# Performance work log

Hardware: AMD Instinct MI355X
Metric: run time of the kernel (lower is better)

## Reference

```python
import jax, jax.numpy as jnp
import numpy as np

H = 128          # hidden_dim
L = 3            # n_layers
G = 128          # num graphs in batch
BN_EPS = 1e-5


def setup_inputs() -> dict:
    key = jax.random.key(0)
    ks = jax.random.split(key, 16)
    N, E, ND, ED = 2048, 8192, 32, 16
    s = lambda k, shape, fan: jax.random.normal(k, shape, dtype=jnp.float32) / np.sqrt(fan)
    return {
        "x": jax.random.normal(ks[0], (N, ND), dtype=jnp.float32),
        "edge_index": jax.random.randint(ks[1], (2, E), 0, N),
        "edge_attr": jax.random.normal(ks[2], (E, ED), dtype=jnp.float32),
        "batch": jnp.sort(jax.random.randint(ks[3], (N,), 0, G)),
        "node_W": s(ks[4], (ND, H), ND),
        "node_b": jnp.zeros((H,), jnp.float32),
        "edge_W": s(ks[5], (L, ED, H * H), ED),
        "edge_b": jnp.zeros((L, H * H), jnp.float32),
        "root_W": s(ks[6], (L, H, H), H),
        "conv_bias": jnp.zeros((L, H), jnp.float32),
        "bn_gamma": jnp.ones((L, H), jnp.float32),
        "bn_beta": jnp.zeros((L, H), jnp.float32),
        "cls_W1": s(ks[7], (H, 64), H),
        "cls_b1": jnp.zeros((64,), jnp.float32),
        "cls_W2": s(ks[8], (64, 1), 64),
        "cls_b2": jnp.zeros((1,), jnp.float32),
    }


def _segment_mean(vals, ids, num_segments):
    ssum = jax.ops.segment_sum(vals, ids, num_segments=num_segments)
    cnt = jax.ops.segment_sum(jnp.ones((vals.shape[0],), vals.dtype), ids,
                              num_segments=num_segments)
    return ssum / jnp.maximum(cnt, 1.0)[:, None]


def reference(x, edge_index, edge_attr, batch, node_W, node_b, edge_W, edge_b,
              root_W, conv_bias, bn_gamma, bn_beta, cls_W1, cls_b1, cls_W2, cls_b2):
    N = x.shape[0]
    src, dst = edge_index[0], edge_index[1]
    h = x @ node_W + node_b                                   # [N, H]
    for l in range(L):
        # edge-conditioned weights: [E, H, H]
        W = (edge_attr @ edge_W[l] + edge_b[l]).reshape(-1, H, H)
        msg = jnp.einsum('ei,eio->eo', h[src], W)             # gather + per-edge matmul
        agg = _segment_mean(msg, dst, N)                      # scatter-mean
        x_new = h @ root_W[l] + agg + conv_bias[l]
        # BatchNorm (batch statistics, training-mode math)
        mu = jnp.mean(x_new, axis=0)
        var = jnp.var(x_new, axis=0)
        x_new = (x_new - mu) * jax.lax.rsqrt(var + BN_EPS) * bn_gamma[l] + bn_beta[l]
        x_new = jax.nn.relu(x_new)                            # dropout omitted (eval)
        h = h + x_new                                         # residual
    g = _segment_mean(h, batch, G)                            # global mean pool [G, H]
    out = jax.nn.relu(g @ cls_W1 + cls_b1) @ cls_W2 + cls_b2  # classifier
    return out.squeeze(-1)                                    # [G]
```

## Files before the change

kernel.cpp:

```cpp
#include <hip/hip_runtime.h>
#include <cstddef>
#include <cstdint>

#define H 128
#define EDIM 16
#define NLAYER 3
#define NSLICE 18
#define WCOLS (NSLICE * H)
#define PCOLS (EDIM * H)
#define TM 64
#define TN 64
#define TK 16

typedef unsigned short ushort_t;
typedef unsigned int uint_t;
typedef __attribute__((ext_vector_type(8))) short bf16x8;
typedef __attribute__((ext_vector_type(4))) float f32x4;

__device__ __forceinline__ ushort_t f2bf(float f) {
    uint_t u = __builtin_bit_cast(uint_t, f);
    u += 0x7fffu + ((u >> 16) & 1u);
    return (ushort_t)(u >> 16);
}
__device__ __forceinline__ float bf_lo(uint_t u) {
    return __builtin_bit_cast(float, u << 16);
}
__device__ __forceinline__ float bf_hi(uint_t u) {
    return __builtin_bit_cast(float, u & 0xffff0000u);
}

__global__ __launch_bounds__(256) void setup_kernel(
    const int* __restrict__ dst, const int* __restrict__ batch,
    int* __restrict__ hist, float* __restrict__ cntG, int E, int N,
    const float* __restrict__ eW, const float* __restrict__ eb,
    const float* __restrict__ rW, ushort_t* __restrict__ Wt)
{
    if (blockIdx.x < 32) {
        int t = blockIdx.x * 256 + threadIdx.x;
        if (t < E) atomicAdd(&hist[dst[t]], 1);
        if (t < N) atomicAdd(&cntG[batch[t]], 1.f);
        return;
    }
    __shared__ ushort_t tile[128][136];
    const int b = blockIdx.x - 32;
    const int l = b / NSLICE, s = b % NSLICE;
    const float* S = (s < 16) ? (eW + ((size_t)l * 16 + s) * (H * H))
                   : (s == 16 ? (eb + (size_t)l * H * H)
                              : (rW + (size_t)l * H * H));
    const int t = threadIdx.x;
    const int k = t >> 1, o0 = (t & 1) * 64;
#pragma unroll
    for (int j = 0; j < 64; j += 4) {
        float4 v = *(const float4*)&S[(size_t)k * H + o0 + j];
        tile[k][o0 + j + 0] = f2bf(v.x);
        tile[k][o0 + j + 1] = f2bf(v.y);
        tile[k][o0 + j + 2] = f2bf(v.z);
        tile[k][o0 + j + 3] = f2bf(v.w);
    }
    __syncthreads();
    const int n = t >> 1, k0 = (t & 1) * 64;
    ushort_t* outp = Wt + ((size_t)l * WCOLS + s * H + n) * H + k0;
#pragma unroll 8
    for (int j = 0; j < 64; ++j) outp[j] = tile[k0 + j][n];
}

__global__ __launch_bounds__(256) void scan_kernel(
    const int* __restrict__ hist, int* __restrict__ offs, int N)
{
    __shared__ int part[256];
    const int t = threadIdx.x;
    const int base = t * 8;
    int v[8], loc[8], s = 0;
#pragma unroll
    for (int j = 0; j < 8; ++j) v[j] = hist[base + j];
#pragma unroll
    for (int j = 0; j < 8; ++j) { loc[j] = s; s += v[j]; }
    part[t] = s;
    __syncthreads();
    for (int off = 1; off < 256; off <<= 1) {
        int x = (t >= off) ? part[t - off] : 0;
        __syncthreads();
        part[t] += x;
        __syncthreads();
    }
    const int boff = (t == 0) ? 0 : part[t - 1];
#pragma unroll
    for (int j = 0; j < 8; ++j) offs[base + j] = boff + loc[j];
    if (t == 255) offs[N] = boff + s;
}

__global__ void scatter_kernel(const int* __restrict__ dst,
                               const int* __restrict__ offs,
                               int* __restrict__ fill, int* __restrict__ eord, int E)
{
    const int e = blockIdx.x * 256 + threadIdx.x;
    if (e >= E) return;
    const int d = dst[e];
    const int pos = offs[d] + atomicAdd(&fill[d], 1);
    eord[pos] = e;
}

__global__ __launch_bounds__(256) void gemm_embed(
    const float* __restrict__ A, const float* __restrict__ B,
    const float* __restrict__ bias, float* __restrict__ C,
    ushort_t* __restrict__ Cbf, int M, int K, int N)
{
    __shared__ float As[TK][TM + 4];
    __shared__ float Bs[TK][TN + 4];
    const int bm = blockIdx.y * TM;
    const int bn = blockIdx.x * TN;
    const int tid = threadIdx.x;
    const int tx = tid & 15;
    const int ty = tid >> 4;

    float acc[4][4];
#pragma unroll
    for (int i = 0; i < 4; ++i)
#pragma unroll
        for (int j = 0; j < 4; ++j) acc[i][j] = 0.f;

    const int ka = tid & 15, ma = tid >> 4;
    const int nb = tid & 63, kb = tid >> 6;

    for (int k0 = 0; k0 < K; k0 += TK) {
#pragma unroll
        for (int r = 0; r < 4; ++r)
            As[ka][ma + 16 * r] = A[(size_t)(bm + ma + 16 * r) * K + (k0 + ka)];
#pragma unroll
        for (int r = 0; r < 4; ++r)
            Bs[kb + 4 * r][nb] = B[(size_t)(k0 + kb + 4 * r) * N + bn + nb];
        __syncthreads();
#pragma unroll
        for (int kk = 0; kk < TK; ++kk) {
            const float4 a4 = *(const float4*)&As[kk][ty * 4];
            const float4 b4 = *(const float4*)&Bs[kk][tx * 4];
            const float a[4] = {a4.x, a4.y, a4.z, a4.w};
            const float b[4] = {b4.x, b4.y, b4.z, b4.w};
#pragma unroll
            for (int i = 0; i < 4; ++i)
#pragma unroll
                for (int j = 0; j < 4; ++j)
                    acc[i][j] = fmaf(a[i], b[j], acc[i][j]);
        }
        __syncthreads();
    }

#pragma unroll
    for (int i = 0; i < 4; ++i) {
        const int row = bm + ty * 4 + i;
        float4 v;
        v.x = acc[i][0] + bias[(bn + tx * 4 + 0) & 127];
        v.y = acc[i][1] + bias[(bn + tx * 4 + 1) & 127];
        v.z = acc[i][2] + bias[(bn + tx * 4 + 2) & 127];
        v.w = acc[i][3] + bias[(bn + tx * 4 + 3) & 127];
        *(float4*)&C[(size_t)row * N + bn + tx * 4] = v;
        ushort_t* o = &Cbf[(size_t)row * N + bn + tx * 4];
        o[0] = f2bf(v.x); o[1] = f2bf(v.y); o[2] = f2bf(v.z); o[3] = f2bf(v.w);
    }
}

__global__ __launch_bounds__(256) void mfma_gemm(
    const ushort_t* __restrict__ hbf, const ushort_t* __restrict__ Wt,
    ushort_t* __restrict__ Pb, float* __restrict__ QR)
{
    __shared__ ushort_t As[64][136];
    __shared__ ushort_t Bs[64][136];
    const int tid = threadIdx.x;
    const int v0 = blockIdx.y * 64;
    const int n0 = blockIdx.x * 64;

    {
        const int row = tid >> 2, col0 = (tid & 3) * 32;
        const ushort_t* ga = hbf + (size_t)(v0 + row) * H + col0;
        const ushort_t* gb = Wt + (size_t)(n0 + row) * H + col0;
#pragma unroll
        for (int j = 0; j < 32; j += 8) {
            *(uint4*)&As[row][col0 + j] = *(const uint4*)(ga + j);
            *(uint4*)&Bs[row][col0 + j] = *(const uint4*)(gb + j);
        }
    }
    __syncthreads();

    const int wave = tid >> 6, lane = tid & 63;
    const int l15 = lane & 15, kg = lane >> 4;
    const int mrow = wave * 16 + l15;

    f32x4 acc0 = {0.f, 0.f, 0.f, 0.f};
    f32x4 acc1 = {0.f, 0.f, 0.f, 0.f};
    f32x4 acc2 = {0.f, 0.f, 0.f, 0.f};
    f32x4 acc3 = {0.f, 0.f, 0.f, 0.f};

#pragma unroll
    for (int s = 0; s < 4; ++s) {
        const int k = s * 32 + kg * 8;
        bf16x8 a = *(const bf16x8*)&As[mrow][k];
        bf16x8 b0 = *(const bf16x8*)&Bs[0 * 16 + l15][k];
        bf16x8 b1 = *(const bf16x8*)&Bs[1 * 16 + l15][k];
        bf16x8 b2 = *(const bf16x8*)&Bs[2 * 16 + l15][k];
        bf16x8 b3 = *(const bf16x8*)&Bs[3 * 16 + l15][k];
        acc0 = __builtin_amdgcn_mfma_f32_16x16x32_bf16(a, b0, acc0, 0, 0, 0);
        acc1 = __builtin_amdgcn_mfma_f32_16x16x32_bf16(a, b1, acc1, 0, 0, 0);
        acc2 = __builtin_amdgcn_mfma_f32_16x16x32_bf16(a, b2, acc2, 0, 0, 0);
        acc3 = __builtin_amdgcn_mfma_f32_16x16x32_bf16(a, b3, acc3, 0, 0, 0);
    }

    const int slice = n0 >> 7;
    const int lo = n0 & 127;
    const int row0 = v0 + wave * 16 + kg * 4;
    if (slice < 16) {
        ushort_t* op = Pb + (size_t)row0 * PCOLS + slice * H + lo + l15;
#pragma unroll
        for (int r = 0; r < 4; ++r) {
            op[(size_t)r * PCOLS + 0]  = f2bf(acc0[r]);
            op[(size_t)r * PCOLS + 16] = f2bf(acc1[r]);
            op[(size_t)r * PCOLS + 32] = f2bf(acc2[r]);
            op[(size_t)r * PCOLS + 48] = f2bf(acc3[r]);
        }
    } else {
        float* op = QR + (size_t)row0 * 256 + (slice - 16) * H + lo + l15;
#pragma unroll
        for (int r = 0; r < 4; ++r) {
            op[(size_t)r * 256 + 0]  = acc0[r];
            op[(size_t)r * 256 + 16] = acc1[r];
            op[(size_t)r * 256 + 32] = acc2[r];
            op[(size_t)r * 256 + 48] = acc3[r];
        }
    }
}

__global__ __launch_bounds__(256) void edge_stats(
    const ushort_t* __restrict__ Pb, const float* __restrict__ QR,
    const float* __restrict__ ea, const int* __restrict__ srcArr,
    const int* __restrict__ offs, const int* __restrict__ hist,
    const int* __restrict__ eord, const float* __restrict__ conv_b,
    float* __restrict__ xnew, float* __restrict__ bnS, float* __restrict__ bnQ)
{
    __shared__ float sS[4][H];
    __shared__ float sQ[4][H];
    const int tid = threadIdx.x;
    const int sb = tid >> 6;
    const int o2 = tid & 63;
    const int v = blockIdx.x * 4 + sb;

    const int st = offs[v];
    const int deg = hist[v];
    float m0 = 0.f, m1 = 0.f;
    for (int k = 0; k < deg; ++k) {
        const int e = eord[st + k];
        const int s = srcArr[e];
        const float* eap = ea + (size_t)e * EDIM;
        const float4 w0 = *(const float4*)(eap + 0);
        const float4 w1 = *(const float4*)(eap + 4);
        const float4 w2 = *(const float4*)(eap + 8);
        const float4 w3 = *(const float4*)(eap + 12);
        const float w[16] = {w0.x, w0.y, w0.z, w0.w, w1.x, w1.y, w1.z, w1.w,
                             w2.x, w2.y, w2.z, w2.w, w3.x, w3.y, w3.z, w3.w};
        const uint_t* prow = (const uint_t*)(Pb + (size_t)s * PCOLS) + o2;
        const float2 q2 = *(const float2*)(QR + (size_t)s * 256 + 2 * o2);
        m0 += q2.x;
        m1 += q2.y;
#pragma unroll
        for (int d = 0; d < EDIM; ++d) {
            const uint_t u = prow[(size_t)d * 64];
            m0 = fmaf(w[d], bf_lo(u), m0);
            m1 = fmaf(w[d], bf_hi(u), m1);
        }
    }
    const float rc = 1.0f / (float)(deg > 0 ? deg : 1);
    const float2 rt = *(const float2*)(QR + (size_t)v * 256 + H + 2 * o2);
    const float2 cb = *(const float2*)(conv_b + 2 * o2);
    const float val0 = m0 * rc + rt.x + cb.x;
    const float val1 = m1 * rc + rt.y + cb.y;
    *(float2*)(xnew + (size_t)v * H + 2 * o2) = make_float2(val0, val1);
    sS[sb][2 * o2] = val0; sS[sb][2 * o2 + 1] = val1;
    sQ[sb][2 * o2] = val0 * val0; sQ[sb][2 * o2 + 1] = val1 * val1;
    __syncthreads();
    if (tid < H) {
        const float s4 = sS[0][tid] + sS[1][tid] + sS[2][tid] + sS[3][tid];
        const float q4 = sQ[0][tid] + sQ[1][tid] + sQ[2][tid] + sQ[3][tid];
        atomicAdd(&bnS[tid], s4);
        atomicAdd(&bnQ[tid], q4);
    }
}

__global__ __launch_bounds__(256) void bn_apply(
    float* __restrict__ h, ushort_t* __restrict__ hbf,
    const float* __restrict__ xnew,
    const float* __restrict__ bnS, const float* __restrict__ bnQ,
    const float* __restrict__ gamma, const float* __restrict__ beta,
    const int* __restrict__ batch, float* __restrict__ gsum, int N, int last)
{
    const int idx = blockIdx.x * 256 + threadIdx.x;
    const int c = idx & 127;
    const int v = idx >> 7;
    const float invN = 1.0f / (float)N;
    const float mu = bnS[c] * invN;
    const float var = bnQ[c] * invN - mu * mu;
    const float val = (xnew[idx] - mu) * rsqrtf(var + 1e-5f) * gamma[c] + beta[c];
    const float hn = h[idx] + fmaxf(val, 0.f);
    h[idx] = hn;
    hbf[idx] = f2bf(hn);
    if (last) atomicAdd(&gsum[batch[v] * H + c], hn);
}

__global__ void classifier_kernel(
    const float* __restrict__ gsum, const float* __restrict__ cntG,
    const float* __restrict__ W1, const float* __restrict__ b1,
    const float* __restrict__ W2, const float* __restrict__ b2,
    float* __restrict__ out)
{
    const int g = blockIdx.x;
    const int j = threadIdx.x;
    const float rc = 1.0f / fmaxf(cntG[g], 1.0f);
    float acc = b1[j];
#pragma unroll 8
    for (int i = 0; i < H; ++i)
        acc = fmaf(gsum[g * H + i] * rc, W1[i * 64 + j], acc);
    float pv = fmaxf(acc, 0.f) * W2[j];
#pragma unroll
    for (int off = 32; off > 0; off >>= 1)
        pv += __shfl_down(pv, off);
    if (j == 0) out[g] = pv + b2[0];
}

extern "C" void kernel_launch(void* const* d_in, const int* in_sizes, int n_in,
                              void* d_out, int out_size, void* d_ws, size_t ws_size,
                              hipStream_t stream)
{
    const float* x      = (const float*)d_in[0];
    const int*   eidx   = (const int*)  d_in[1];
    const float* eattr  = (const float*)d_in[2];
    const int*   batch  = (const int*)  d_in[3];
    const float* node_W = (const float*)d_in[4];
    const float* node_b = (const float*)d_in[5];
    const float* edge_W = (const float*)d_in[6];
    const float* edge_b = (const float*)d_in[7];
    const float* root_W = (const float*)d_in[8];
    const float* conv_b = (const float*)d_in[9];
    const float* gamma  = (const float*)d_in[10];
    const float* beta   = (const float*)d_in[11];
    const float* W1     = (const float*)d_in[12];
    const float* b1     = (const float*)d_in[13];
    const float* W2     = (const float*)d_in[14];
    const float* b2     = (const float*)d_in[15];
    float* out = (float*)d_out;

    const int N = in_sizes[0] / 32;
    const int E = in_sizes[1] / 2;
    const int G = out_size;

    int* hist   = (int*)d_ws;
    int* fill   = hist + N;
    float* cntG = (float*)(fill + N);
    float* bnS  = cntG + G;
    float* bnQ  = bnS + NLAYER * H;
    float* gsum = bnQ + NLAYER * H;
    int* offs   = (int*)(gsum + (size_t)G * H);
    int* eord   = offs + (N + 16);
    float* h    = (float*)(eord + E);
    float* xnew = h + (size_t)N * H;
    ushort_t* hbf = (ushort_t*)(xnew + (size_t)N * H);
    ushort_t* Wt  = hbf + (size_t)N * H;
    ushort_t* Pb  = Wt + (size_t)NLAYER * WCOLS * H;
    float* QR   = (float*)(Pb + (size_t)N * PCOLS);

    const size_t zbytes = (size_t)(2 * N) * 4
                        + ((size_t)G + 2 * NLAYER * H + (size_t)G * H) * 4;
    hipMemsetAsync(hist, 0, zbytes, stream);

    const int* src = eidx;
    const int* dst = eidx + E;

    setup_kernel<<<32 + NLAYER * NSLICE, 256, 0, stream>>>(
        dst, batch, hist, cntG, E, N, edge_W, edge_b, root_W, Wt);
    scan_kernel<<<1, 256, 0, stream>>>(hist, offs, N);
    scatter_kernel<<<E / 256, 256, 0, stream>>>(dst, offs, fill, eord, E);

    gemm_embed<<<dim3(H / TN, N / TM), 256, 0, stream>>>(
        x, node_W, node_b, h, hbf, N, 32, H);

    for (int l = 0; l < NLAYER; ++l) {
        mfma_gemm<<<dim3(WCOLS / 64, N / 64), 256, 0, stream>>>(
            hbf, Wt + (size_t)l * WCOLS * H, Pb, QR);
        edge_stats<<<N / 4, 256, 0, stream>>>(
            Pb, QR, eattr, src, offs, hist, eord,
            conv_b + (size_t)l * H, xnew, bnS + l * H, bnQ + l * H);
        bn_apply<<<(N * H) / 256, 256, 0, stream>>>(
            h, hbf, xnew, bnS + l * H, bnQ + l * H,
            gamma + (size_t)l * H, beta + (size_t)l * H,
            batch, gsum, N, l == NLAYER - 1);
    }

    classifier_kernel<<<G, 64, 0, stream>>>(gsum, cntG, W1, b1, W2, b2, out);
}
```

Before: 205.7 us.

## Reassociate edge conv as per-node aggregation then single K=2304 GEMM

The per-layer pipeline changes order. Instead of computing h times every edge-weight slice for all nodes and then gathering those products per edge, each node now builds a vector of edge-attribute-weighted sums of its neighbours' h, plus the plain neighbour sum and its own h, all in bf16. That vector is then multiplied once against the concatenated weights, with K=2304, with the BN statistics reduced in the same kernel. The histogram, scan, scatter, embedding GEMM, weight transpose and zeroing are merged into one setup kernel, which removes the memset and several launches. The conv bias is dropped because batch-norm mean subtraction cancels it. Risks: the new GEMM runs only N/16 blocks, each streaming the full weight matrix through an unpipelined K loop, and U is staged as a large bf16 buffer.

```diff
diff --git a/kernel.cpp b/kernel.cpp
--- a/kernel.cpp
+++ b/kernel.cpp
@@ -5,12 +5,8 @@
 #define H 128
 #define EDIM 16
 #define NLAYER 3
+#define KU 2304
 #define NSLICE 18
-#define WCOLS (NSLICE * H)
-#define PCOLS (EDIM * H)
-#define TM 64
-#define TN 64
-#define TK 16
 
 typedef unsigned short ushort_t;
 typedef unsigned int uint_t;
@@ -22,232 +18,174 @@
     u += 0x7fffu + ((u >> 16) & 1u);
     return (ushort_t)(u >> 16);
 }
-__device__ __forceinline__ float bf_lo(uint_t u) {
-    return __builtin_bit_cast(float, u << 16);
-}
-__device__ __forceinline__ float bf_hi(uint_t u) {
-    return __builtin_bit_cast(float, u & 0xffff0000u);
+__device__ __forceinline__ uint_t pack2(float a, float b) {
+    return (uint_t)f2bf(a) | ((uint_t)f2bf(b) << 16);
 }
 
 __global__ __launch_bounds__(256) void setup_kernel(
     const int* __restrict__ dst, const int* __restrict__ batch,
-    int* __restrict__ hist, float* __restrict__ cntG, int E, int N,
+    const float* __restrict__ x, const float* __restrict__ node_W,
+    const float* __restrict__ node_b,
     const float* __restrict__ eW, const float* __restrict__ eb,
-    const float* __restrict__ rW, ushort_t* __restrict__ Wt)
-{
-    if (blockIdx.x < 32) {
-        int t = blockIdx.x * 256 + threadIdx.x;
-        if (t < E) atomicAdd(&hist[dst[t]], 1);
-        if (t < N) atomicAdd(&cntG[batch[t]], 1.f);
+    const float* __restrict__ rW,
+    int* __restrict__ offs, int* __restrict__ deg, int* __restrict__ eord,
+    float* __restrict__ cntG, float* __restrict__ bnS, float* __restrict__ bnQ,
+    float* __restrict__ gsum, float* __restrict__ h, ushort_t* __restrict__ Wt2,
+    int E, int N, int G)
+{
+    alignas(16) __shared__ unsigned char smem[34816];
+    const int b = blockIdx.x;
+    const int t = threadIdx.x;
+    const int NBe = (N / 64) * 2;
+
+    if (b == 0) {
+        int* sh = (int*)smem;
+        int* part = sh + 2048;
+        for (int i = t; i < N; i += 256) sh[i] = 0;
+        __syncthreads();
+        for (int e = t; e < E; e += 256) atomicAdd(&sh[dst[e]], 1);
+        __syncthreads();
+        const int base = t * 8;
+        int v[8], loc[8], s = 0;
+#pragma unroll
+        for (int j = 0; j < 8; ++j) v[j] = (base + j < N) ? sh[base + j] : 0;
+#pragma unroll
+        for (int j = 0; j < 8; ++j) { loc[j] = s; s += v[j]; }
+        part[t] = s;
+        __syncthreads();
+        for (int off = 1; off < 256; off <<= 1) {
+            int xp = (t >= off) ? part[t - off] : 0;
+            __syncthreads();
+            part[t] += xp;
+            __syncthreads();
+        }
+        const int boff = (t == 0) ? 0 : part[t - 1];
+#pragma unroll
+        for (int j = 0; j < 8; ++j) {
+            if (base + j < N) {
+                deg[base + j] = v[j];
+                offs[base + j] = boff + loc[j];
+            }
+        }
+        if (t == 255) offs[N] = boff + s;
+        __syncthreads();
+        for (int i = t; i < N; i += 256) sh[i] = offs[i];
+        __syncthreads();
+        for (int e = t; e < E; e += 256) {
+            const int d = dst[e];
+            const int pos = atomicAdd(&sh[d], 1);
+            eord[pos] = e;
+        }
         return;
     }
-    __shared__ ushort_t tile[128][136];
-    const int b = blockIdx.x - 32;
-    const int l = b / NSLICE, s = b % NSLICE;
-    const float* S = (s < 16) ? (eW + ((size_t)l * 16 + s) * (H * H))
-                   : (s == 16 ? (eb + (size_t)l * H * H)
-                              : (rW + (size_t)l * H * H));
-    const int t = threadIdx.x;
-    const int k = t >> 1, o0 = (t & 1) * 64;
-#pragma unroll
-    for (int j = 0; j < 64; j += 4) {
-        float4 v = *(const float4*)&S[(size_t)k * H + o0 + j];
-        tile[k][o0 + j + 0] = f2bf(v.x);
-        tile[k][o0 + j + 1] = f2bf(v.y);
-        tile[k][o0 + j + 2] = f2bf(v.z);
-        tile[k][o0 + j + 3] = f2bf(v.w);
-    }
-    __syncthreads();
-    const int n = t >> 1, k0 = (t & 1) * 64;
-    ushort_t* outp = Wt + ((size_t)l * WCOLS + s * H + n) * H + k0;
+
+    if (b <= NLAYER * NSLICE) {
+        ushort_t* tile = (ushort_t*)smem;
+        const int bb = b - 1;
+        const int l = bb / NSLICE, s = bb % NSLICE;
+        const float* S = (s < 16) ? (eW + ((size_t)l * 16 + s) * (H * H))
+                       : (s == 16 ? (eb + (size_t)l * H * H)
+                                  : (rW + (size_t)l * H * H));
+        const int k = t >> 1, o0 = (t & 1) * 64;
+#pragma unroll
+        for (int j = 0; j < 64; j += 4) {
+            float4 v = *(const float4*)&S[(size_t)k * H + o0 + j];
+            tile[k * 136 + o0 + j + 0] = f2bf(v.x);
+            tile[k * 136 + o0 + j + 1] = f2bf(v.y);
+            tile[k * 136 + o0 + j + 2] = f2bf(v.z);
+            tile[k * 136 + o0 + j + 3] = f2bf(v.w);
+        }
+        __syncthreads();
+        const int n = t >> 1, k0 = (t & 1) * 64;
+        ushort_t* outp = Wt2 + ((size_t)(l * H + n)) * KU + s * H + k0;
 #pragma unroll 8
-    for (int j = 0; j < 64; ++j) outp[j] = tile[k0 + j][n];
-}
-
-__global__ __launch_bounds__(256) void scan_kernel(
-    const int* __restrict__ hist, int* __restrict__ offs, int N)
-{
-    __shared__ int part[256];
-    const int t = threadIdx.x;
-    const int base = t * 8;
-    int v[8], loc[8], s = 0;
-#pragma unroll
-    for (int j = 0; j < 8; ++j) v[j] = hist[base + j];
-#pragma unroll
-    for (int j = 0; j < 8; ++j) { loc[j] = s; s += v[j]; }
-    part[t] = s;
-    __syncthreads();
-    for (int off = 1; off < 256; off <<= 1) {
-        int x = (t >= off) ? part[t - off] : 0;
-        __syncthreads();
-        part[t] += x;
-        __syncthreads();
-    }
-    const int boff = (t == 0) ? 0 : part[t - 1];
-#pragma unroll
-    for (int j = 0; j < 8; ++j) offs[base + j] = boff + loc[j];
-    if (t == 255) offs[N] = boff + s;
-}
-
-__global__ void scatter_kernel(const int* __restrict__ dst,
-                               const int* __restrict__ offs,
-                               int* __restrict__ fill, int* __restrict__ eord, int E)
-{
-    const int e = blockIdx.x * 256 + threadIdx.x;
-    if (e >= E) return;
-    const int d = dst[e];
-    const int pos = offs[d] + atomicAdd(&fill[d], 1);
-    eord[pos] = e;
-}
-
-__global__ __launch_bounds__(256) void gemm_embed(
-    const float* __restrict__ A, const float* __restrict__ B,
-    const float* __restrict__ bias, float* __restrict__ C,
-    ushort_t* __restrict__ Cbf, int M, int K, int N)
-{
-    __shared__ float As[TK][TM + 4];
-    __shared__ float Bs[TK][TN + 4];
-    const int bm = blockIdx.y * TM;
-    const int bn = blockIdx.x * TN;
-    const int tid = threadIdx.x;
-    const int tx = tid & 15;
-    const int ty = tid >> 4;
-
-    float acc[4][4];
-#pragma unroll
-    for (int i = 0; i < 4; ++i)
-#pragma unroll
-        for (int j = 0; j < 4; ++j) acc[i][j] = 0.f;
-
-    const int ka = tid & 15, ma = tid >> 4;
-    const int nb = tid & 63, kb = tid >> 6;
-
-    for (int k0 = 0; k0 < K; k0 += TK) {
-#pragma unroll
-        for (int r = 0; r < 4; ++r)
-            As[ka][ma + 16 * r] = A[(size_t)(bm + ma + 16 * r) * K + (k0 + ka)];
-#pragma unroll
-        for (int r = 0; r < 4; ++r)
-            Bs[kb + 4 * r][nb] = B[(size_t)(k0 + kb + 4 * r) * N + bn + nb];
-        __syncthreads();
-#pragma unroll
-        for (int kk = 0; kk < TK; ++kk) {
-            const float4 a4 = *(const float4*)&As[kk][ty * 4];
-            const float4 b4 = *(const float4*)&Bs[kk][tx * 4];
-            const float a[4] = {a4.x, a4.y, a4.z, a4.w};
-            const float b[4] = {b4.x, b4.y, b4.z, b4.w};
-#pragma unroll
-            for (int i = 0; i < 4; ++i)
-#pragma unroll
-                for (int j = 0; j < 4; ++j)
-                    acc[i][j] = fmaf(a[i], b[j], acc[i][j]);
-        }
-        __syncthreads();
-    }
-
-#pragma unroll
-    for (int i = 0; i < 4; ++i) {
-        const int row = bm + ty * 4 + i;
-        float4 v;
-        v.x = acc[i][0] + bias[(bn + tx * 4 + 0) & 127];
-        v.y = acc[i][1] + bias[(bn + tx * 4 + 1) & 127];
-        v.z = acc[i][2] + bias[(bn + tx * 4 + 2) & 127];
-        v.w = acc[i][3] + bias[(bn + tx * 4 + 3) & 127];
-        *(float4*)&C[(size_t)row * N + bn + tx * 4] = v;
-        ushort_t* o = &Cbf[(size_t)row * N + bn + tx * 4];
-        o[0] = f2bf(v.x); o[1] = f2bf(v.y); o[2] = f2bf(v.z); o[3] = f2bf(v.w);
-    }
-}
-
-__global__ __launch_bounds__(256) void mfma_gemm(
-    const ushort_t* __restrict__ hbf, const ushort_t* __restrict__ Wt,
-    ushort_t* __restrict__ Pb, float* __restrict__ QR)
-{
-    __shared__ ushort_t As[64][136];
-    __shared__ ushort_t Bs[64][136];
-    const int tid = threadIdx.x;
-    const int v0 = blockIdx.y * 64;
-    const int n0 = blockIdx.x * 64;
+        for (int j = 0; j < 64; ++j) outp[j] = tile[(k0 + j) * 136 + n];
+        return;
+    }
+
+    if (b <= NLAYER * NSLICE + NBe) {
+        float* As = (float*)smem;
+        float* Bs = As + 16 * 68;
+        const int tt = b - (NLAYER * NSLICE + 1);
+        const int bm = (tt >> 1) * 64;
+        const int bn = (tt & 1) * 64;
+        const int tx = t & 15, ty = t >> 4;
+        float acc[4][4];
+#pragma unroll
+        for (int i = 0; i < 4; ++i)
+#pragma unroll
+            for (int j = 0; j < 4; ++j) acc[i][j] = 0.f;
+        const int ka = t & 15, ma = t >> 4;
+        const int nb = t & 63, kb = t >> 6;
+        for (int k0 = 0; k0 < 32; k0 += 16) {
+#pragma unroll
+            for (int r = 0; r < 4; ++r)
+                As[ka * 68 + ma + 16 * r] = x[(size_t)(bm + ma + 16 * r) * 32 + (k0 + ka)];
+#pragma unroll
+            for (int r = 0; r < 4; ++r)
+                Bs[(kb + 4 * r) * 68 + nb] = node_W[(size_t)(k0 + kb + 4 * r) * H + bn + nb];
+            __syncthreads();
+#pragma unroll
+            for (int kk = 0; kk < 16; ++kk) {
+                const float4 a4 = *(const float4*)&As[kk * 68 + ty * 4];
+                const float4 b4 = *(const float4*)&Bs[kk * 68 + tx * 4];
+                const float a[4] = {a4.x, a4.y, a4.z, a4.w};
+                const float bv[4] = {b4.x, b4.y, b4.z, b4.w};
+#pragma unroll
+                for (int i = 0; i < 4; ++i)
+#pragma unroll
+                    for (int j = 0; j < 4; ++j)
+                        acc[i][j] = fmaf(a[i], bv[j], acc[i][j]);
+            }
+            __syncthreads();
+        }
+#pragma unroll
+        for (int i = 0; i < 4; ++i) {
+            const int row = bm + ty * 4 + i;
+            float4 v;
+            v.x = acc[i][0] + node_b[bn + tx * 4 + 0];
+            v.y = acc[i][1] + node_b[bn + tx * 4 + 1];
+            v.z = acc[i][2] + node_b[bn + tx * 4 + 2];
+            v.w = acc[i][3] + node_b[bn + tx * 4 + 3];
+            *(float4*)&h[(size_t)row * H + bn + tx * 4] = v;
+        }
+        return;
+    }
 
     {
-        const int row = tid >> 2, col0 = (tid & 3) * 32;
-        const ushort_t* ga = hbf + (size_t)(v0 + row) * H + col0;
-        const ushort_t* gb = Wt + (size_t)(n0 + row) * H + col0;
-#pragma unroll
-        for (int j = 0; j < 32; j += 8) {
-            *(uint4*)&As[row][col0 + j] = *(const uint4*)(ga + j);
-            *(uint4*)&Bs[row][col0 + j] = *(const uint4*)(gb + j);
-        }
-    }
-    __syncthreads();
-
-    const int wave = tid >> 6, lane = tid & 63;
-    const int l15 = lane & 15, kg = lane >> 4;
-    const int mrow = wave * 16 + l15;
-
-    f32x4 acc0 = {0.f, 0.f, 0.f, 0.f};
-    f32x4 acc1 = {0.f, 0.f, 0.f, 0.f};
-    f32x4 acc2 = {0.f, 0.f, 0.f, 0.f};
-    f32x4 acc3 = {0.f, 0.f, 0.f, 0.f};
-
-#pragma unroll
-    for (int s = 0; s < 4; ++s) {
-        const int k = s * 32 + kg * 8;
-        bf16x8 a = *(const bf16x8*)&As[mrow][k];
-        bf16x8 b0 = *(const bf16x8*)&Bs[0 * 16 + l15][k];
-        bf16x8 b1 = *(const bf16x8*)&Bs[1 * 16 + l15][k];
-        bf16x8 b2 = *(const bf16x8*)&Bs[2 * 16 + l15][k];
-        bf16x8 b3 = *(const bf16x8*)&Bs[3 * 16 + l15][k];
-        acc0 = __builtin_amdgcn_mfma_f32_16x16x32_bf16(a, b0, acc0, 0, 0, 0);
-        acc1 = __builtin_amdgcn_mfma_f32_16x16x32_bf16(a, b1, acc1, 0, 0, 0);
-        acc2 = __builtin_amdgcn_mfma_f32_16x16x32_bf16(a, b2, acc2, 0, 0, 0);
-        acc3 = __builtin_amdgcn_mfma_f32_16x16x32_bf16(a, b3, acc3, 0, 0, 0);
-    }
-
-    const int slice = n0 >> 7;
-    const int lo = n0 & 127;
-    const int row0 = v0 + wave * 16 + kg * 4;
-    if (slice < 16) {
-        ushort_t* op = Pb + (size_t)row0 * PCOLS + slice * H + lo + l15;
-#pragma unroll
-        for (int r = 0; r < 4; ++r) {
-            op[(size_t)r * PCOLS + 0]  = f2bf(acc0[r]);
-            op[(size_t)r * PCOLS + 16] = f2bf(acc1[r]);
-            op[(size_t)r * PCOLS + 32] = f2bf(acc2[r]);
-            op[(size_t)r * PCOLS + 48] = f2bf(acc3[r]);
-        }
-    } else {
-        float* op = QR + (size_t)row0 * 256 + (slice - 16) * H + lo + l15;
-#pragma unroll
-        for (int r = 0; r < 4; ++r) {
-            op[(size_t)r * 256 + 0]  = acc0[r];
-            op[(size_t)r * 256 + 16] = acc1[r];
-            op[(size_t)r * 256 + 32] = acc2[r];
-            op[(size_t)r * 256 + 48] = acc3[r];
-        }
-    }
-}
-
-__global__ __launch_bounds__(256) void edge_stats(
-    const ushort_t* __restrict__ Pb, const float* __restrict__ QR,
-    const float* __restrict__ ea, const int* __restrict__ srcArr,
-    const int* __restrict__ offs, const int* __restrict__ hist,
-    const int* __restrict__ eord, const float* __restrict__ conv_b,
-    float* __restrict__ xnew, float* __restrict__ bnS, float* __restrict__ bnQ)
-{
-    __shared__ float sS[4][H];
-    __shared__ float sQ[4][H];
+        const int zcount = G * H + 2 * NLAYER * H + G;
+        for (int i = t; i < zcount; i += 256) {
+            if (i < G * H) gsum[i] = 0.f;
+            else if (i < G * H + NLAYER * H) bnS[i - G * H] = 0.f;
+            else if (i < G * H + 2 * NLAYER * H) bnQ[i - G * H - NLAYER * H] = 0.f;
+            else cntG[i - G * H - 2 * NLAYER * H] = 0.f;
+        }
+        __syncthreads();
+        for (int v = t; v < N; v += 256) atomicAdd(&cntG[batch[v]], 1.f);
+    }
+}
+
+__global__ __launch_bounds__(256) void ubuild_kernel(
+    const float* __restrict__ h, const float* __restrict__ ea,
+    const int* __restrict__ src, const int* __restrict__ offs,
+    const int* __restrict__ deg, const int* __restrict__ eord,
+    ushort_t* __restrict__ Ub, int N)
+{
     const int tid = threadIdx.x;
     const int sb = tid >> 6;
-    const int o2 = tid & 63;
+    const int j = tid & 63;
     const int v = blockIdx.x * 4 + sb;
+    if (v >= N) return;
+
+    float u[17][2];
+#pragma unroll
+    for (int d = 0; d < 17; ++d) { u[d][0] = 0.f; u[d][1] = 0.f; }
 
     const int st = offs[v];
-    const int deg = hist[v];
-    float m0 = 0.f, m1 = 0.f;
-    for (int k = 0; k < deg; ++k) {
+    const int dg = deg[v];
+    for (int k = 0; k < dg; ++k) {
         const int e = eord[st + k];
-        const int s = srcArr[e];
+        const int s = src[e];
         const float* eap = ea + (size_t)e * EDIM;
         const float4 w0 = *(const float4*)(eap + 0);
         const float4 w1 = *(const float4*)(eap + 4);
@@ -255,37 +193,89 @@
         const float4 w3 = *(const float4*)(eap + 12);
         const float w[16] = {w0.x, w0.y, w0.z, w0.w, w1.x, w1.y, w1.z, w1.w,
                              w2.x, w2.y, w2.z, w2.w, w3.x, w3.y, w3.z, w3.w};
-        const uint_t* prow = (const uint_t*)(Pb + (size_t)s * PCOLS) + o2;
-        const float2 q2 = *(const float2*)(QR + (size_t)s * 256 + 2 * o2);
-        m0 += q2.x;
-        m1 += q2.y;
-#pragma unroll
-        for (int d = 0; d < EDIM; ++d) {
-            const uint_t u = prow[(size_t)d * 64];
-            m0 = fmaf(w[d], bf_lo(u), m0);
-            m1 = fmaf(w[d], bf_hi(u), m1);
-        }
-    }
-    const float rc = 1.0f / (float)(deg > 0 ? deg : 1);
-    const float2 rt = *(const float2*)(QR + (size_t)v * 256 + H + 2 * o2);
-    const float2 cb = *(const float2*)(conv_b + 2 * o2);
-    const float val0 = m0 * rc + rt.x + cb.x;
-    const float val1 = m1 * rc + rt.y + cb.y;
-    *(float2*)(xnew + (size_t)v * H + 2 * o2) = make_float2(val0, val1);
-    sS[sb][2 * o2] = val0; sS[sb][2 * o2 + 1] = val1;
-    sQ[sb][2 * o2] = val0 * val0; sQ[sb][2 * o2 + 1] = val1 * val1;
-    __syncthreads();
-    if (tid < H) {
-        const float s4 = sS[0][tid] + sS[1][tid] + sS[2][tid] + sS[3][tid];
-        const float q4 = sQ[0][tid] + sQ[1][tid] + sQ[2][tid] + sQ[3][tid];
-        atomicAdd(&bnS[tid], s4);
-        atomicAdd(&bnQ[tid], q4);
+        const float2 h2 = *(const float2*)&h[(size_t)s * H + 2 * j];
+        u[16][0] += h2.x;
+        u[16][1] += h2.y;
+#pragma unroll
+        for (int d = 0; d < 16; ++d) {
+            u[d][0] = fmaf(w[d], h2.x, u[d][0]);
+            u[d][1] = fmaf(w[d], h2.y, u[d][1]);
+        }
+    }
+    const float rc = 1.0f / (float)(dg > 0 ? dg : 1);
+    uint_t* outp = (uint_t*)(Ub + (size_t)v * KU) + j;
+#pragma unroll
+    for (int d = 0; d < 17; ++d)
+        outp[(size_t)d * 64] = pack2(u[d][0] * rc, u[d][1] * rc);
+    const float2 hv = *(const float2*)&h[(size_t)v * H + 2 * j];
+    outp[(size_t)17 * 64] = pack2(hv.x, hv.y);
+}
+
+__global__ __launch_bounds__(256) void gemm_stats(
+    const ushort_t* __restrict__ Ub, const ushort_t* __restrict__ Wt2l,
+    float* __restrict__ xnew, float* __restrict__ bnS, float* __restrict__ bnQ)
+{
+    __shared__ ushort_t As[16][136];
+    __shared__ ushort_t Bs[128][136];
+    const int tid = threadIdx.x;
+    const int m0 = blockIdx.x * 16;
+    const int wave = tid >> 6, lane = tid & 63;
+    const int l15 = lane & 15, quad = lane >> 4;
+
+    f32x4 acc0 = {0.f, 0.f, 0.f, 0.f};
+    f32x4 acc1 = {0.f, 0.f, 0.f, 0.f};
+
+    for (int c = 0; c < KU / 128; ++c) {
+        {
+            const int row = tid >> 4, pos = (tid & 15) * 8;
+            *(uint4*)&As[row][pos] =
+                *(const uint4*)&Ub[(size_t)(m0 + row) * KU + c * 128 + pos];
+        }
+#pragma unroll
+        for (int r = 0; r < 8; ++r) {
+            const int idx = tid + r * 256;
+            const int row = idx >> 4, pos = (idx & 15) * 8;
+            *(uint4*)&Bs[row][pos] =
+                *(const uint4*)&Wt2l[(size_t)row * KU + c * 128 + pos];
+        }
+        __syncthreads();
+#pragma unroll
+        for (int ks = 0; ks < 4; ++ks) {
+            const int k = ks * 32 + quad * 8;
+            bf16x8 a  = *(const bf16x8*)&As[l15][k];
+            bf16x8 b0 = *(const bf16x8*)&Bs[wave * 16 + l15][k];
+            bf16x8 b1 = *(const bf16x8*)&Bs[(wave + 4) * 16 + l15][k];
+            acc0 = __builtin_amdgcn_mfma_f32_16x16x32_bf16(a, b0, acc0, 0, 0, 0);
+            acc1 = __builtin_amdgcn_mfma_f32_16x16x32_bf16(a, b1, acc1, 0, 0, 0);
+        }
+        __syncthreads();
+    }
+
+    float s0 = 0.f, q0 = 0.f, s1 = 0.f, q1 = 0.f;
+#pragma unroll
+    for (int r = 0; r < 4; ++r) {
+        const int row = m0 + quad * 4 + r;
+        const float v0 = acc0[r];
+        const float v1 = acc1[r];
+        xnew[(size_t)row * H + wave * 16 + l15] = v0;
+        xnew[(size_t)row * H + (wave + 4) * 16 + l15] = v1;
+        s0 += v0; q0 += v0 * v0;
+        s1 += v1; q1 += v1 * v1;
+    }
+    s0 += __shfl_down(s0, 32); s0 += __shfl_down(s0, 16);
+    q0 += __shfl_down(q0, 32); q0 += __shfl_down(q0, 16);
+    s1 += __shfl_down(s1, 32); s1 += __shfl_down(s1, 16);
+    q1 += __shfl_down(q1, 32); q1 += __shfl_down(q1, 16);
+    if (quad == 0) {
+        atomicAdd(&bnS[wave * 16 + l15], s0);
+        atomicAdd(&bnQ[wave * 16 + l15], q0);
+        atomicAdd(&bnS[(wave + 4) * 16 + l15], s1);
+        atomicAdd(&bnQ[(wave + 4) * 16 + l15], q1);
     }
 }
 
 __global__ __launch_bounds__(256) void bn_apply(
-    float* __restrict__ h, ushort_t* __restrict__ hbf,
-    const float* __restrict__ xnew,
+    float* __restrict__ h, const float* __restrict__ xnew,
     const float* __restrict__ bnS, const float* __restrict__ bnQ,
     const float* __restrict__ gamma, const float* __restrict__ beta,
     const int* __restrict__ batch, float* __restrict__ gsum, int N, int last)
@@ -299,7 +289,6 @@
     const float val = (xnew[idx] - mu) * rsqrtf(var + 1e-5f) * gamma[c] + beta[c];
     const float hn = h[idx] + fmaxf(val, 0.f);
     h[idx] = hn;
-    hbf[idx] = f2bf(hn);
     if (last) atomicAdd(&gsum[batch[v] * H + c], hn);
 }
 
@@ -336,7 +325,6 @@
     const float* edge_W = (const float*)d_in[6];
     const float* edge_b = (const float*)d_in[7];
     const float* root_W = (const float*)d_in[8];
-    const float* conv_b = (const float*)d_in[9];
     const float* gamma  = (const float*)d_in[10];
     const float* beta   = (const float*)d_in[11];
     const float* W1     = (const float*)d_in[12];
@@ -349,44 +337,35 @@
     const int E = in_sizes[1] / 2;
     const int G = out_size;
 
-    int* hist   = (int*)d_ws;
-    int* fill   = hist + N;
-    float* cntG = (float*)(fill + N);
+    const int* src = eidx;
+    const int* dst = eidx + E;
+
+    int* offs  = (int*)d_ws;
+    int* deg   = offs + (N + 16);
+    int* eord  = deg + N;
+    float* cntG = (float*)(eord + E);
     float* bnS  = cntG + G;
     float* bnQ  = bnS + NLAYER * H;
     float* gsum = bnQ + NLAYER * H;
-    int* offs   = (int*)(gsum + (size_t)G * H);
-    int* eord   = offs + (N + 16);
-    float* h    = (float*)(eord + E);
+    float* h    = gsum + (size_t)G * H;
     float* xnew = h + (size_t)N * H;
-    ushort_t* hbf = (ushort_t*)(xnew + (size_t)N * H);
-    ushort_t* Wt  = hbf + (size_t)N * H;
-    ushort_t* Pb  = Wt + (size_t)NLAYER * WCOLS * H;
-    float* QR   = (float*)(Pb + (size_t)N * PCOLS);
-
-    const size_t zbytes = (size_t)(2 * N) * 4
-                        + ((size_t)G + 2 * NLAYER * H + (size_t)G * H) * 4;
-    hipMemsetAsync(hist, 0, zbytes, stream);
-
-    const int* src = eidx;
-    const int* dst = eidx + E;
-
-    setup_kernel<<<32 + NLAYER * NSLICE, 256, 0, stream>>>(
-        dst, batch, hist, cntG, E, N, edge_W, edge_b, root_W, Wt);
-    scan_kernel<<<1, 256, 0, stream>>>(hist, offs, N);
-    scatter_kernel<<<E / 256, 256, 0, stream>>>(dst, offs, fill, eord, E);
-
-    gemm_embed<<<dim3(H / TN, N / TM), 256, 0, stream>>>(
-        x, node_W, node_b, h, hbf, N, 32, H);
+    ushort_t* Wt2 = (ushort_t*)(xnew + (size_t)N * H);
+    ushort_t* Ub  = Wt2 + (size_t)NLAYER * H * KU;
+
+    const int NBe = (N / 64) * 2;
+    const int nsetup = 1 + NLAYER * NSLICE + NBe + 1;
+
+    setup_kernel<<<nsetup, 256, 0, stream>>>(
+        dst, batch, x, node_W, node_b, edge_W, edge_b, root_W,
+        offs, deg, eord, cntG, bnS, bnQ, gsum, h, Wt2, E, N, G);
 
     for (int l = 0; l < NLAYER; ++l) {
-        mfma_gemm<<<dim3(WCOLS / 64, N / 64), 256, 0, stream>>>(
-            hbf, Wt + (size_t)l * WCOLS * H, Pb, QR);
-        edge_stats<<<N / 4, 256, 0, stream>>>(
-            Pb, QR, eattr, src, offs, hist, eord,
-            conv_b + (size_t)l * H, xnew, bnS + l * H, bnQ + l * H);
+        ubuild_kernel<<<N / 4, 256, 0, stream>>>(
+            h, eattr, src, offs, deg, eord, Ub, N);
+        gemm_stats<<<N / 16, 256, 0, stream>>>(
+            Ub, Wt2 + (size_t)l * H * KU, xnew, bnS + l * H, bnQ + l * H);
         bn_apply<<<(N * H) / 256, 256, 0, stream>>>(
-            h, hbf, xnew, bnS + l * H, bnQ + l * H,
+            h, xnew, bnS + l * H, bnQ + l * H,
             gamma + (size_t)l * H, beta + (size_t)l * H,
             batch, gsum, N, l == NLAYER - 1);
     }
```

Result: slower. 224.9 us (+9.3%).
